# Kernel optimization log

Measured on AMD Instinct MI355X. Metric: run time of the kernel, lower is better.

Reference implementation:

```python
import jax, jax.numpy as jnp
import numpy as np

B, S, E, H, FF = 4, 2048, 1024, 16, 4096
DK = E // H
EPS = 1e-5


def setup_inputs() -> dict:
    key = jax.random.key(0)
    ks = jax.random.split(key, 16)
    sc = 0.02
    return {
        "x": jax.random.normal(ks[0], (B, S, E), jnp.float32),
        "Wq": jax.random.normal(ks[1], (E, E), jnp.float32) * sc,
        "Wk": jax.random.normal(ks[2], (E, E), jnp.float32) * sc,
        "Wv": jax.random.normal(ks[3], (E, E), jnp.float32) * sc,
        "Wo": jax.random.normal(ks[4], (E, E), jnp.float32) * sc,
        "theta": jax.random.normal(ks[5], (DK,), jnp.float32),
        "Wcq": jax.random.normal(ks[6], (E, E), jnp.float32) * sc,
        "ln1_g": jnp.ones((E,), jnp.float32),
        "ln1_b": jnp.zeros((E,), jnp.float32),
        "W1": jax.random.normal(ks[7], (E, FF), jnp.float32) * sc,
        "b1": jnp.zeros((FF,), jnp.float32),
        "W2": jax.random.normal(ks[8], (FF, E), jnp.float32) * sc,
        "b2": jnp.zeros((E,), jnp.float32),
        "ln2_g": jnp.ones((E,), jnp.float32),
        "ln2_b": jnp.zeros((E,), jnp.float32),
    }


def _layernorm(x, g, b):
    mu = jnp.mean(x, axis=-1, keepdims=True)
    var = jnp.mean(jnp.square(x - mu), axis=-1, keepdims=True)
    return (x - mu) * jax.lax.rsqrt(var + EPS) * g + b


def reference(x, Wq, Wk, Wv, Wo, theta, Wcq, ln1_g, ln1_b, W1, b1, W2, b2, ln2_g, ln2_b):
    mix = 0.5
    # classical multi-head attention
    def heads(t):  # [B,S,E] -> [B,H,S,DK]
        return t.reshape(B, S, H, DK).transpose(0, 2, 1, 3)
    q = heads(x @ Wq)
    k = heads(x @ Wk)
    v = heads(x @ Wv)
    scores = jnp.einsum("bhqd,bhkd->bhqk", q, k) / jnp.sqrt(jnp.float32(DK))
    attn = jax.nn.softmax(scores, axis=-1)
    ctx = jnp.einsum("bhqk,bhkd->bhqd", attn, v)
    ctx = ctx.transpose(0, 2, 1, 3).reshape(B, S, E)
    classical = ctx @ Wo
    # quantum heads: RX(x)RX(theta)|0>, <Z> = cos(x + theta), same theta shared per head
    qh = jnp.cos(x.reshape(B, S, H, DK) + theta)  # broadcast over wires
    quantum = qh.reshape(B, S, E) @ Wcq
    attn_out = mix * classical + (1.0 - mix) * quantum
    x1 = _layernorm(x + attn_out, ln1_g, ln1_b)
    ffn = jax.nn.relu(x1 @ W1 + b1) @ W2 + b2
    return _layernorm(x1 + ffn, ln2_g, ln2_b)
```

## Files before the change

kernel.cpp:

```cpp
#include <hip/hip_runtime.h>
#include <hip/hip_bf16.h>

typedef __bf16 bf16_t;
typedef bf16_t bf16x8 __attribute__((ext_vector_type(8)));
typedef bf16_t bf16x4v __attribute__((ext_vector_type(4)));
typedef float f32x4 __attribute__((ext_vector_type(4)));

static constexpr int EE = 1024;
static constexpr int SS = 2048;
static constexpr int DK = 64;
static constexpr float QSCALE = 0.125f * 1.44269504f;

__device__ __forceinline__ void gload_lds16(const void* g, void* l) {
  __builtin_amdgcn_global_load_lds(
      (__attribute__((address_space(1))) void*)g,
      (__attribute__((address_space(3))) void*)l, 16, 0, 0);
}

__device__ __forceinline__ f32x4 mfma16(bf16x8 a, bf16x8 b, f32x4 c) {
  return __builtin_amdgcn_mfma_f32_16x16x32_bf16(a, b, c, 0, 0, 0);
}

__global__ void __launch_bounds__(256) prep_x_kernel(
    const float* __restrict__ x, const float* __restrict__ theta,
    bf16_t* __restrict__ xbf, bf16_t* __restrict__ A2)
{
  const long t = (long)blockIdx.x * 256 + threadIdx.x;
  const long e0 = t * 8;
  const int col = (int)(e0 & (EE - 1));
  const long row = e0 >> 10;
  const float4 v0 = *(const float4*)&x[e0];
  const float4 v1 = *(const float4*)&x[e0 + 4];
  float xs[8] = {v0.x, v0.y, v0.z, v0.w, v1.x, v1.y, v1.z, v1.w};
  const int d0 = col & (DK - 1);
  bf16x8 xb, qb;
#pragma unroll
  for (int j = 0; j < 8; ++j) {
    xb[j] = (bf16_t)xs[j];
    qb[j] = (bf16_t)__cosf(xs[j] + theta[d0 + j]);
  }
  *(bf16x8*)&xbf[e0] = xb;
  *(bf16x8*)&A2[row * 2048 + EE + col] = qb;
}

__global__ void __launch_bounds__(256) transpose_w_kernel(
    const float* __restrict__ src, bf16_t* __restrict__ dst,
    int N, long dstride, long dcol0)
{
  __shared__ float tile[32][33];
  const int tx = threadIdx.x, ty = threadIdx.y;
  const long n0 = (long)blockIdx.x * 32, k0 = (long)blockIdx.y * 32;
#pragma unroll
  for (int j = 0; j < 4; ++j)
    tile[ty + j * 8][tx] = src[(k0 + ty + j * 8) * N + n0 + tx];
  __syncthreads();
#pragma unroll
  for (int j = 0; j < 4; ++j)
    dst[(n0 + ty + j * 8) * dstride + dcol0 + k0 + tx] = (bf16_t)tile[tx][ty + j * 8];
}

template<int MODE, int TN>
__global__ void __launch_bounds__(512, 2) gemm256(
    const bf16_t* __restrict__ A, const bf16_t* __restrict__ Bt,
    void* __restrict__ C, int M, int N, int K,
    const float* __restrict__ aux1, const bf16_t* __restrict__ aux2)
{
  constexpr int NB = TN / 64;
  __shared__ bf16_t As[4][256 * 32];
  __shared__ bf16_t Bs[4][TN * 32];
  const int tid = threadIdx.x;
  const int lane = tid & 63, wid = tid >> 6;
  const int wr = wid >> 2, wc = wid & 3;
  const int lr = lane & 15, lk = lane >> 4;
  const int gx = gridDim.x;
  const int nwg = gx * gridDim.y;
  const int bid = blockIdx.y * gx + blockIdx.x;
  const int swz = (bid & 7) * (nwg >> 3) + (bid >> 3);
  const long m0 = (long)(swz / gx) * 256;
  const long n0 = (long)(swz % gx) * TN;

  const int rql = lane >> 2;
  const int sl  = lane & 3;
  const int rA0 = wid * 32 + rql, rA1 = wid * 32 + 16 + rql;
  const bf16_t* sA0 = &A [(m0 + rA0) * K + 8 * (sl ^ ((rA0 >> 1) & 3))];
  const bf16_t* sA1 = &A [(m0 + rA1) * K + 8 * (sl ^ ((rA1 >> 1) & 3))];
  const int rB0 = (TN == 256) ? (wid * 32 + rql) : (wid * 16 + rql);
  const int rB1 = wid * 32 + 16 + rql;
  const bf16_t* sB0 = &Bt[(n0 + rB0) * K + 8 * (sl ^ ((rB0 >> 1) & 3))];
  const bf16_t* sB1 = &Bt[(n0 + rB1) * K + 8 * (sl ^ ((rB1 >> 1) & 3))];
  const int loA = wid * 1024;
  const int loB = (TN == 256) ? wid * 1024 : wid * 512;

  f32x4 acc[8][NB] = {};
  const int NKT = K / 32;

  auto stA = [&](int t) {
    const int s = t & 3;
    gload_lds16(sA0 + (long)t * 32, &As[s][loA]);
    gload_lds16(sA1 + (long)t * 32, &As[s][loA + 512]);
  };
  auto stB = [&](int t) {
    const int s = t & 3;
    gload_lds16(sB0 + (long)t * 32, &Bs[s][loB]);
    if constexpr (TN == 256)
      gload_lds16(sB1 + (long)t * 32, &Bs[s][loB + 512]);
  };

  stA(0); stB(0); stA(1); stB(1); stA(2); stB(2);
  if constexpr (TN == 256) { asm volatile("s_waitcnt vmcnt(8)" ::: "memory"); }
  else                     { asm volatile("s_waitcnt vmcnt(6)" ::: "memory"); }
  __builtin_amdgcn_s_barrier();

  for (int t = 0; t < NKT; ++t) {
    const int s = t & 3;
    bf16x8 bfr[NB], af[4];
#pragma unroll
    for (int nb = 0; nb < NB; ++nb) {
      const int rw = wc * (TN / 4) + nb * 16 + lr;
      bfr[nb] = *(const bf16x8*)&Bs[s][rw * 32 + (lk ^ ((rw >> 1) & 3)) * 8];
    }
#pragma unroll
    for (int mb = 0; mb < 4; ++mb) {
      const int rw = wr * 128 + mb * 16 + lr;
      af[mb] = *(const bf16x8*)&As[s][rw * 32 + (lk ^ ((rw >> 1) & 3)) * 8];
    }
    if (t + 3 < NKT) stA(t + 3);
    asm volatile("s_waitcnt lgkmcnt(0)" ::: "memory");
    __builtin_amdgcn_sched_barrier(0);
    __builtin_amdgcn_s_setprio(1);
#pragma unroll
    for (int mb = 0; mb < 4; ++mb)
#pragma unroll
      for (int nb = 0; nb < NB; ++nb)
        acc[mb][nb] = mfma16(af[mb], bfr[nb], acc[mb][nb]);
    __builtin_amdgcn_s_setprio(0);
#pragma unroll
    for (int mb = 0; mb < 4; ++mb) {
      const int rw = wr * 128 + 64 + mb * 16 + lr;
      af[mb] = *(const bf16x8*)&As[s][rw * 32 + (lk ^ ((rw >> 1) & 3)) * 8];
    }
    if (t + 3 < NKT) stB(t + 3);
    asm volatile("s_waitcnt lgkmcnt(0)" ::: "memory");
    __builtin_amdgcn_sched_barrier(0);
    __builtin_amdgcn_s_setprio(1);
#pragma unroll
    for (int mb = 0; mb < 4; ++mb)
#pragma unroll
      for (int nb = 0; nb < NB; ++nb)
        acc[mb + 4][nb] = mfma16(af[mb], bfr[nb], acc[mb + 4][nb]);
    __builtin_amdgcn_s_setprio(0);
    if (t + 3 < NKT) {
      if constexpr (TN == 256) { asm volatile("s_waitcnt vmcnt(8)" ::: "memory"); }
      else                     { asm volatile("s_waitcnt vmcnt(6)" ::: "memory"); }
    } else if (t + 3 == NKT) {
      if constexpr (TN == 256) { asm volatile("s_waitcnt vmcnt(4)" ::: "memory"); }
      else                     { asm volatile("s_waitcnt vmcnt(3)" ::: "memory"); }
    } else if (t + 2 == NKT) {
      asm volatile("s_waitcnt vmcnt(0)" ::: "memory");
    }
    __builtin_amdgcn_s_barrier();
  }

#pragma unroll
  for (int mb = 0; mb < 8; ++mb)
#pragma unroll
    for (int nb = 0; nb < NB; ++nb)
#pragma unroll
      for (int i = 0; i < 4; ++i) {
        const long r = m0 + wr * 128 + mb * 16 + lk * 4 + i;
        const long cc = n0 + wc * (TN / 4) + nb * 16 + lr;
        float v = acc[mb][nb][i];
        if constexpr (MODE == 0) {
          if (cc < 1024) v *= QSCALE;
          ((bf16_t*)C)[r * N + cc] = (bf16_t)v;
        } else if constexpr (MODE == 1) {
          ((float*)C)[r * N + cc] = 0.5f * v + aux1[r * N + cc];
        } else if constexpr (MODE == 2) {
          ((bf16_t*)C)[r * N + cc] = (bf16_t)fmaxf(v + aux1[cc], 0.0f);
        } else {
          ((float*)C)[r * N + cc] = v + aux1[cc] + (float)aux2[r * N + cc];
        }
      }
}

__global__ void __launch_bounds__(256, 2) attn_kernel(
    const bf16_t* __restrict__ QKV, bf16_t* __restrict__ Ctx)
{
  __shared__ bf16_t Ks[2][64 * 72];
  __shared__ bf16_t Vt[2][64 * 72];
  const int tid = threadIdx.x;
  const int lane = tid & 63, w = tid >> 6;
  const int lr = lane & 15, lk = lane >> 4;
  const int bh = blockIdx.x, b = bh >> 4, h = bh & 15;
  const long rowbase = (long)b * SS;
  const int q0 = blockIdx.y * 128;
  const int qcol = h * 64, kcol = EE + h * 64, vcol = 2 * EE + h * 64;
  constexpr int NT = SS / 64;

  bf16x8 qf[2][2];
#pragma unroll
  for (int mb = 0; mb < 2; ++mb)
#pragma unroll
    for (int ks = 0; ks < 2; ++ks)
      qf[mb][ks] = *(const bf16x8*)&QKV[
          (rowbase + q0 + w * 32 + mb * 16 + lr) * 3072 + qcol + ks * 32 + lk * 8];

  const int sr = tid >> 3;
  const int g  = tid & 7;
  const int d0 = g * 8;

  bf16x8 kreg[2], vreg[2];
  auto load_kv = [&](int t) {
#pragma unroll
    for (int it = 0; it < 2; ++it) {
      const long r = rowbase + (long)t * 64 + sr + it * 32;
      kreg[it] = *(const bf16x8*)&QKV[r * 3072 + kcol + d0];
      vreg[it] = *(const bf16x8*)&QKV[r * 3072 + vcol + d0];
    }
  };
  auto write_kv = [&](int buf) {
#pragma unroll
    for (int it = 0; it < 2; ++it) {
      const int r = sr + it * 32;
      *(bf16x8*)&Ks[buf][r * 72 + d0] = kreg[it];
      const int sg = (r & 0x23) | ((r & 0x0C) << 1) | ((r & 0x10) >> 2);
      const int vbase = d0 * 72 + (((sg >> 3) + g) & 7) * 8 + (sg & 7);
#pragma unroll
      for (int jj = 0; jj < 8; ++jj)
        Vt[buf][vbase + jj * 72] = vreg[it][jj];
    }
  };

  f32x4 oacc[2][4] = {};
  float lsum[2] = {0.0f, 0.0f};

  load_kv(0);
  write_kv(0);

  for (int t = 0; t < NT; ++t) {
    const int buf = t & 1;
    if (t + 1 < NT) load_kv(t + 1);
    __syncthreads();

    bf16x8 kf[4][2];
#pragma unroll
    for (int nb = 0; nb < 4; ++nb)
#pragma unroll
      for (int ks = 0; ks < 2; ++ks)
        kf[nb][ks] = *(const bf16x8*)&Ks[buf][(nb * 16 + lr) * 72 + ks * 32 + lk * 8];

    f32x4 sacc[2][4] = {};
    __builtin_amdgcn_s_setprio(1);
#pragma unroll
    for (int mb = 0; mb < 2; ++mb)
#pragma unroll
      for (int nb = 0; nb < 4; ++nb)
#pragma unroll
        for (int ks = 0; ks < 2; ++ks)
          sacc[mb][nb] = mfma16(kf[nb][ks], qf[mb][ks], sacc[mb][nb]);
    __builtin_amdgcn_s_setprio(0);

    bf16x8 vf[4][2];
#pragma unroll
    for (int nb = 0; nb < 4; ++nb)
#pragma unroll
      for (int ks = 0; ks < 2; ++ks) {
        const int dvr = nb * 16 + lr;
        vf[nb][ks] = *(const bf16x8*)&Vt[buf][dvr * 72 + (((ks * 4 + lk) + (dvr >> 3)) & 7) * 8];
      }

#pragma unroll
    for (int mb = 0; mb < 2; ++mb) {
      float psum = 0.0f;
      bf16x8 pf[2];
#pragma unroll
      for (int nb = 0; nb < 4; ++nb)
#pragma unroll
        for (int i = 0; i < 4; ++i) {
          const float pv = exp2f(sacc[mb][nb][i]);
          psum += pv;
          pf[nb >> 1][(nb & 1) * 4 + i] = (bf16_t)pv;
        }
      lsum[mb] += psum;
      __builtin_amdgcn_s_setprio(1);
#pragma unroll
      for (int nb = 0; nb < 4; ++nb)
#pragma unroll
        for (int ks = 0; ks < 2; ++ks)
          oacc[mb][nb] = mfma16(pf[ks], vf[nb][ks], oacc[mb][nb]);
      __builtin_amdgcn_s_setprio(0);
    }

    if (t + 1 < NT) write_kv((t + 1) & 1);
  }

#pragma unroll
  for (int mb = 0; mb < 2; ++mb) {
    float l = lsum[mb];
    l += __shfl_xor(l, 16);
    l += __shfl_xor(l, 32);
    float li[4];
#pragma unroll
    for (int i = 0; i < 4; ++i) li[i] = 1.0f / __shfl(l, lk * 4 + i);
#pragma unroll
    for (int nb = 0; nb < 4; ++nb)
#pragma unroll
      for (int i = 0; i < 4; ++i) {
        const long r = rowbase + q0 + w * 32 + mb * 16 + lk * 4 + i;
        Ctx[r * 2048 + h * 64 + nb * 16 + lr] = (bf16_t)(oacc[mb][nb][i] * li[i]);
      }
  }
}

__device__ __forceinline__ void ln_reduce(const float4& v, int tid,
                                          float& mu, float& rs) {
  float s = v.x + v.y + v.z + v.w;
  float ss = v.x * v.x + v.y * v.y + v.z * v.z + v.w * v.w;
#pragma unroll
  for (int off = 1; off < 64; off <<= 1) {
    s += __shfl_xor(s, off);
    ss += __shfl_xor(ss, off);
  }
  __shared__ float wsum[4], wsq[4];
  if ((tid & 63) == 0) { wsum[tid >> 6] = s; wsq[tid >> 6] = ss; }
  __syncthreads();
  s = wsum[0] + wsum[1] + wsum[2] + wsum[3];
  ss = wsq[0] + wsq[1] + wsq[2] + wsq[3];
  mu = s * (1.0f / EE);
  rs = rsqrtf(ss * (1.0f / EE) - mu * mu + 1e-5f);
}

__global__ void __launch_bounds__(256) ln_bf16_kernel(
    const float* __restrict__ pre, const float* __restrict__ g,
    const float* __restrict__ bt, bf16_t* __restrict__ out)
{
  const int r = blockIdx.x, tid = threadIdx.x;
  const long base = (long)r * EE + tid * 4;
  const float4 v = *(const float4*)&pre[base];
  float mu, rs;
  ln_reduce(v, tid, mu, rs);
  const float4 gv = *(const float4*)&g[tid * 4];
  const float4 bv = *(const float4*)&bt[tid * 4];
  bf16x4v o;
  o[0] = (bf16_t)((v.x - mu) * rs * gv.x + bv.x);
  o[1] = (bf16_t)((v.y - mu) * rs * gv.y + bv.y);
  o[2] = (bf16_t)((v.z - mu) * rs * gv.z + bv.z);
  o[3] = (bf16_t)((v.w - mu) * rs * gv.w + bv.w);
  *(bf16x4v*)&out[base] = o;
}

__global__ void __launch_bounds__(256) ln_f32_kernel(
    const float* __restrict__ pre, const float* __restrict__ g,
    const float* __restrict__ bt, float* __restrict__ out)
{
  const int r = blockIdx.x, tid = threadIdx.x;
  const long base = (long)r * EE + tid * 4;
  const float4 v = *(const float4*)&pre[base];
  float mu, rs;
  ln_reduce(v, tid, mu, rs);
  const float4 gv = *(const float4*)&g[tid * 4];
  const float4 bv = *(const float4*)&bt[tid * 4];
  float4 o;
  o.x = (v.x - mu) * rs * gv.x + bv.x;
  o.y = (v.y - mu) * rs * gv.y + bv.y;
  o.z = (v.z - mu) * rs * gv.z + bv.z;
  o.w = (v.w - mu) * rs * gv.w + bv.w;
  *(float4*)&out[base] = o;
}

extern "C" void kernel_launch(void* const* d_in, const int* in_sizes, int n_in,
                              void* d_out, int out_size, void* d_ws, size_t ws_size,
                              hipStream_t stream)
{
  (void)in_sizes; (void)n_in; (void)out_size; (void)ws_size;
  const float* x     = (const float*)d_in[0];
  const float* Wq    = (const float*)d_in[1];
  const float* Wk    = (const float*)d_in[2];
  const float* Wv    = (const float*)d_in[3];
  const float* Wo    = (const float*)d_in[4];
  const float* theta = (const float*)d_in[5];
  const float* Wcq   = (const float*)d_in[6];
  const float* ln1g  = (const float*)d_in[7];
  const float* ln1b  = (const float*)d_in[8];
  const float* W1    = (const float*)d_in[9];
  const float* b1    = (const float*)d_in[10];
  const float* W2    = (const float*)d_in[11];
  const float* b2    = (const float*)d_in[12];
  const float* ln2g  = (const float*)d_in[13];
  const float* ln2b  = (const float*)d_in[14];

  char* ws = (char*)d_ws;
  const size_t MB = 1ull << 20;
  bf16_t* xbf    = (bf16_t*)(ws + 0);
  bf16_t* QKV    = (bf16_t*)(ws + 16 * MB);
  float*  preLN1 = (float*)(ws + 16 * MB);
  bf16_t* A2     = (bf16_t*)(ws + 64 * MB);
  float*  preLN2 = (float*)(ws + 64 * MB);
  bf16_t* H1     = (bf16_t*)(ws + 96 * MB);
  bf16_t* BtQKV  = (bf16_t*)(ws + 160 * MB);
  bf16_t* Bt2    = (bf16_t*)(ws + 166 * MB);
  bf16_t* BtW1   = (bf16_t*)(ws + 170 * MB);
  bf16_t* BtW2   = (bf16_t*)(ws + 178 * MB);

  dim3 tb(32, 8);
  prep_x_kernel<<<4096, 256, 0, stream>>>(x, theta, xbf, A2);
  transpose_w_kernel<<<dim3(32, 32), tb, 0, stream>>>(Wq,  BtQKV,              1024, 1024, 0);
  transpose_w_kernel<<<dim3(32, 32), tb, 0, stream>>>(Wk,  BtQKV + 1024*1024,  1024, 1024, 0);
  transpose_w_kernel<<<dim3(32, 32), tb, 0, stream>>>(Wv,  BtQKV + 2048*1024,  1024, 1024, 0);
  transpose_w_kernel<<<dim3(32, 32), tb, 0, stream>>>(Wo,  Bt2,  1024, 2048, 0);
  transpose_w_kernel<<<dim3(32, 32), tb, 0, stream>>>(Wcq, Bt2,  1024, 2048, 1024);
  transpose_w_kernel<<<dim3(128, 32), tb, 0, stream>>>(W1, BtW1, 4096, 1024, 0);
  transpose_w_kernel<<<dim3(32, 128), tb, 0, stream>>>(W2, BtW2, 1024, 4096, 0);

  gemm256<0, 256><<<dim3(12, 32), 512, 0, stream>>>(xbf, BtQKV, QKV, 8192, 3072, 1024, nullptr, nullptr);
  attn_kernel<<<dim3(64, 16), 256, 0, stream>>>(QKV, A2);
  gemm256<1, 128><<<dim3(8, 32), 512, 0, stream>>>(A2, Bt2, preLN1, 8192, 1024, 2048, x, nullptr);
  ln_bf16_kernel<<<8192, 256, 0, stream>>>(preLN1, ln1g, ln1b, xbf);
  gemm256<2, 256><<<dim3(16, 32), 512, 0, stream>>>(xbf, BtW1, H1, 8192, 4096, 1024, b1, nullptr);
  gemm256<3, 128><<<dim3(8, 32), 512, 0, stream>>>(H1, BtW2, preLN2, 8192, 1024, 4096, b2, xbf);
  ln_f32_kernel<<<8192, 256, 0, stream>>>(preLN2, ln2g, ln2b, (float*)d_out);
}
```

Before: 474.4 us.

## Retile TN=128 GEMM warps to 4x2 layout and restructure LDS read pipelining

For TN=128 the GEMM now arranges its 8 waves as 4 rows by 2 columns, each wave computing 64x64 instead of 128x32. This cuts redundant A-fragment LDS reads per MFMA. Both halves of the A fragments are now loaded up front, and the global A and B prefetches are issued together. A partial lgkmcnt wait lets the first MFMA half start while the second half's LDS reads are still in flight. In the attention kernel the barrier moves before the next K/V global load, which changes how that load overlaps with the barrier.

```diff
diff --git a/kernel.cpp b/kernel.cpp
--- a/kernel.cpp
+++ b/kernel.cpp
@@ -65,12 +65,15 @@
     void* __restrict__ C, int M, int N, int K,
     const float* __restrict__ aux1, const bf16_t* __restrict__ aux2)
 {
-  constexpr int NB = TN / 64;
+  constexpr int MB  = (TN == 256) ? 8 : 4;
+  constexpr int MBH = MB / 2;
+  constexpr int NB  = 4;
   __shared__ bf16_t As[4][256 * 32];
   __shared__ bf16_t Bs[4][TN * 32];
   const int tid = threadIdx.x;
   const int lane = tid & 63, wid = tid >> 6;
-  const int wr = wid >> 2, wc = wid & 3;
+  const int wr = (TN == 256) ? (wid >> 2) : (wid >> 1);
+  const int wc = (TN == 256) ? (wid & 3) : (wid & 1);
   const int lr = lane & 15, lk = lane >> 4;
   const int gx = gridDim.x;
   const int nwg = gx * gridDim.y;
@@ -91,7 +94,7 @@
   const int loA = wid * 1024;
   const int loB = (TN == 256) ? wid * 1024 : wid * 512;
 
-  f32x4 acc[8][NB] = {};
+  f32x4 acc[MB][NB] = {};
   const int NKT = K / 32;
 
   auto stA = [&](int t) {
@@ -113,41 +116,42 @@
 
   for (int t = 0; t < NKT; ++t) {
     const int s = t & 3;
-    bf16x8 bfr[NB], af[4];
+    bf16x8 bfr[NB], af1[MBH], af2[MBH];
 #pragma unroll
     for (int nb = 0; nb < NB; ++nb) {
-      const int rw = wc * (TN / 4) + nb * 16 + lr;
+      const int rw = wc * 64 + nb * 16 + lr;
       bfr[nb] = *(const bf16x8*)&Bs[s][rw * 32 + (lk ^ ((rw >> 1) & 3)) * 8];
     }
 #pragma unroll
-    for (int mb = 0; mb < 4; ++mb) {
-      const int rw = wr * 128 + mb * 16 + lr;
-      af[mb] = *(const bf16x8*)&As[s][rw * 32 + (lk ^ ((rw >> 1) & 3)) * 8];
-    }
-    if (t + 3 < NKT) stA(t + 3);
+    for (int mb = 0; mb < MBH; ++mb) {
+      const int rw = wr * (MB * 16) + mb * 16 + lr;
+      af1[mb] = *(const bf16x8*)&As[s][rw * 32 + (lk ^ ((rw >> 1) & 3)) * 8];
+    }
+    __builtin_amdgcn_sched_barrier(0);
+#pragma unroll
+    for (int mb = 0; mb < MBH; ++mb) {
+      const int rw = wr * (MB * 16) + (MBH + mb) * 16 + lr;
+      af2[mb] = *(const bf16x8*)&As[s][rw * 32 + (lk ^ ((rw >> 1) & 3)) * 8];
+    }
+    if (t + 3 < NKT) { stA(t + 3); stB(t + 3); }
+    if constexpr (MBH == 4) { asm volatile("s_waitcnt lgkmcnt(4)" ::: "memory"); }
+    else                    { asm volatile("s_waitcnt lgkmcnt(2)" ::: "memory"); }
+    __builtin_amdgcn_sched_barrier(0);
+    __builtin_amdgcn_s_setprio(1);
+#pragma unroll
+    for (int mb = 0; mb < MBH; ++mb)
+#pragma unroll
+      for (int nb = 0; nb < NB; ++nb)
+        acc[mb][nb] = mfma16(af1[mb], bfr[nb], acc[mb][nb]);
+    __builtin_amdgcn_s_setprio(0);
     asm volatile("s_waitcnt lgkmcnt(0)" ::: "memory");
     __builtin_amdgcn_sched_barrier(0);
     __builtin_amdgcn_s_setprio(1);
 #pragma unroll
-    for (int mb = 0; mb < 4; ++mb)
+    for (int mb = 0; mb < MBH; ++mb)
 #pragma unroll
       for (int nb = 0; nb < NB; ++nb)
-        acc[mb][nb] = mfma16(af[mb], bfr[nb], acc[mb][nb]);
-    __builtin_amdgcn_s_setprio(0);
-#pragma unroll
-    for (int mb = 0; mb < 4; ++mb) {
-      const int rw = wr * 128 + 64 + mb * 16 + lr;
-      af[mb] = *(const bf16x8*)&As[s][rw * 32 + (lk ^ ((rw >> 1) & 3)) * 8];
-    }
-    if (t + 3 < NKT) stB(t + 3);
-    asm volatile("s_waitcnt lgkmcnt(0)" ::: "memory");
-    __builtin_amdgcn_sched_barrier(0);
-    __builtin_amdgcn_s_setprio(1);
-#pragma unroll
-    for (int mb = 0; mb < 4; ++mb)
-#pragma unroll
-      for (int nb = 0; nb < NB; ++nb)
-        acc[mb + 4][nb] = mfma16(af[mb], bfr[nb], acc[mb + 4][nb]);
+        acc[MBH + mb][nb] = mfma16(af2[mb], bfr[nb], acc[MBH + mb][nb]);
     __builtin_amdgcn_s_setprio(0);
     if (t + 3 < NKT) {
       if constexpr (TN == 256) { asm volatile("s_waitcnt vmcnt(8)" ::: "memory"); }
@@ -162,13 +166,13 @@
   }
 
 #pragma unroll
-  for (int mb = 0; mb < 8; ++mb)
+  for (int mb = 0; mb < MB; ++mb)
 #pragma unroll
     for (int nb = 0; nb < NB; ++nb)
 #pragma unroll
       for (int i = 0; i < 4; ++i) {
-        const long r = m0 + wr * 128 + mb * 16 + lk * 4 + i;
-        const long cc = n0 + wc * (TN / 4) + nb * 16 + lr;
+        const long r = m0 + wr * (MB * 16) + mb * 16 + lk * 4 + i;
+        const long cc = n0 + wc * 64 + nb * 16 + lr;
         float v = acc[mb][nb][i];
         if constexpr (MODE == 0) {
           if (cc < 1024) v *= QSCALE;
@@ -239,8 +243,8 @@
 
   for (int t = 0; t < NT; ++t) {
     const int buf = t & 1;
+    __syncthreads();
     if (t + 1 < NT) load_kv(t + 1);
-    __syncthreads();
 
     bf16x8 kf[4][2];
 #pragma unroll
```

After: 454.7 us. 4.2% less time.
